# Kernel tuning notes

Hardware: AMD Instinct MI355X
Metric: run time of the kernel (lower is better)

## Reference

```python
import jax, jax.numpy as jnp
import numpy as np

B, N = 8, 1024
NFEAT, NHID, NHEADS, NCLASS, NLAYERS = 256, 64, 8, 256, 2
ALPHA = 0.2  # LeakyReLU slope inside GAT layers
OUTER_SLOPE = 0.01  # F.leaky_relu default on concatenated heads
NEG = -9e15


def setup_inputs() -> dict:
    key = jax.random.key(0)
    ks = jax.random.split(key, 8)
    x = jax.random.normal(ks[0], (B, N, NFEAT), jnp.float32)
    adj = jax.random.randint(ks[1], (B, N, N), 0, 2).astype(jnp.int32)
    mask = jax.random.randint(ks[2], (B, N), 0, 2).astype(jnp.int32)
    W_att = (jax.random.normal(ks[3], (NHEADS, NFEAT, NHID), jnp.float32) * 0.05)
    a_att = (jax.random.normal(ks[4], (NHEADS, 2 * NHID), jnp.float32) * 0.05)
    W_out = (jax.random.normal(ks[5], (NHID * NHEADS, NCLASS), jnp.float32) * 0.05)
    a_out = (jax.random.normal(ks[6], (2 * NCLASS,), jnp.float32) * 0.05)
    ln_w = jnp.ones((NCLASS,), jnp.float32)
    ln_b = jnp.zeros((NCLASS,), jnp.float32)
    return {"x": x, "adj": adj, "mask": mask, "W_att": W_att, "a_att": a_att,
            "W_out": W_out, "a_out": a_out, "ln_w": ln_w, "ln_b": ln_b}


def _layernorm(x, w, b):
    mu = jnp.mean(x, axis=-1, keepdims=True)
    var = jnp.mean(jnp.square(x - mu), axis=-1, keepdims=True)
    return (x - mu) * jax.lax.rsqrt(var + 1e-5) * w + b


def _gat_forward(x, adj_pos, maskb, W_att, a_att, W_out, a_out, ln_w, ln_b):
    for _ in range(NLAYERS):
        # multi-head GAT layers (concat=True): e_ij = leakyrelu(f1_i + f2_j)
        h = jnp.einsum('bnf,hfo->bhno', x, W_att)            # [B,H,N,F]
        f1 = jnp.einsum('bhno,ho->bhn', h, a_att[:, :NHID])  # [B,H,N]
        f2 = jnp.einsum('bhno,ho->bhn', h, a_att[:, NHID:])
        e = jax.nn.leaky_relu(f1[:, :, :, None] + f2[:, :, None, :], ALPHA)
        att = jax.nn.softmax(jnp.where(adj_pos[:, None], e, NEG), axis=-1)
        hp = jax.nn.elu(jnp.einsum('bhnm,bhmo->bhno', att, h))
        y = jax.nn.leaky_relu(
            hp.transpose(0, 2, 1, 3).reshape(B, N, NHEADS * NHID), OUTER_SLOPE)
        # out attention layer (concat=False)
        ho = y @ W_out                                        # [B,N,C]
        g1 = ho @ a_out[:NCLASS]                              # [B,N]
        g2 = ho @ a_out[NCLASS:]
        eo = jax.nn.leaky_relu(g1[:, :, None] + g2[:, None, :], ALPHA)
        ao = jax.nn.softmax(jnp.where(adj_pos, eo, NEG), axis=-1)
        x = x + jax.nn.elu(jnp.einsum('bnm,bmo->bno', ao, ho))
        x = jnp.where(maskb, 0.0, x)
        x = _layernorm(x, ln_w, ln_b)
    return jax.nn.relu(x), jax.nn.relu(x[:, 0, :])


def reference(x, adj, mask, W_att, a_att, W_out, a_out, ln_w, ln_b):
    adj_pos = adj > 0
    maskb = (mask == 0)[:, :, None]
    return _gat_forward(x, adj_pos, maskb, W_att, a_att, W_out, a_out, ln_w, ln_b)
```

## Files before the change

### kernel.cpp

```cpp
#include <hip/hip_runtime.h>
#include <hip/hip_bf16.h>
#include <math.h>

#define BB 8
#define NN 1024
#define FF 256
#define HH 8
#define OO 64
#define CC 256

typedef __attribute__((ext_vector_type(8))) short short8;
typedef __attribute__((ext_vector_type(4))) short s16x4;
typedef __attribute__((ext_vector_type(4))) float f32x4;
typedef unsigned long long u64;

__device__ __forceinline__ short bf16s(float f) {
    __hip_bfloat16 h = __float2bfloat16(f);
    return *reinterpret_cast<short*>(&h);
}

__global__ void k_prep(const int* __restrict__ adj, const float* __restrict__ x,
                       const float* __restrict__ Wa, const float* __restrict__ Wo,
                       u64* __restrict__ adjbit, __hip_bfloat16* __restrict__ xbf,
                       __hip_bfloat16* __restrict__ WaT, __hip_bfloat16* __restrict__ WoT) {
    int bid = blockIdx.x, t = threadIdx.x;
    if (bid < 32768) {
        int i = bid * 256 + t;
        u64 m = __ballot(adj[i] > 0);
        if ((t & 63) == 0) adjbit[i >> 6] = m;
    } else if (bid < 32768 + 8192) {
        int i = (bid - 32768) * 256 + t;
        xbf[i] = __float2bfloat16(x[i]);
    } else {
        int i = (bid - 32768 - 8192) * 256 + t;
        if (i < 131072) {
            int hd = i >> 14, o = (i >> 8) & 63, f = i & 255;
            WaT[i] = __float2bfloat16(Wa[hd * 16384 + f * 64 + o]);
        } else {
            int j = i - 131072;
            int c = j >> 9, k = j & 511;
            WoT[j] = __float2bfloat16(Wo[k * 256 + c]);
        }
    }
}

__global__ void k_proj_mfma(const __hip_bfloat16* __restrict__ xbf,
                            const __hip_bfloat16* __restrict__ WaT,
                            const float* __restrict__ aatt,
                            __hip_bfloat16* __restrict__ hF,
                            float* __restrict__ f1, float* __restrict__ f2) {
    int tile = blockIdx.x, hd = blockIdx.y;
    int t = threadIdx.x, lane = t & 63, w = t >> 6;
    int r0 = tile * 64;
    int b = r0 >> 10;
    int n0 = r0 & 1023;
    int bh = b * HH + hd;
    int al = lane & 15, ah = lane >> 4;
    const __hip_bfloat16* xrow = xbf + (size_t)(r0 + w * 16 + al) * FF;
    const __hip_bfloat16* Wb = WaT + (size_t)hd * OO * FF;
    f32x4 z4 = {0.f, 0.f, 0.f, 0.f};
    f32x4 acc[4] = {z4, z4, z4, z4};
    for (int k0 = 0; k0 < FF; k0 += 32) {
        int k = k0 + ah * 8;
        short8 af = *(const short8*)&xrow[k];
#pragma unroll
        for (int cf = 0; cf < 4; ++cf) {
            int col = cf * 16 + al;
            short8 bf = *(const short8*)&Wb[(size_t)col * FF + k];
            acc[cf] = __builtin_amdgcn_mfma_f32_16x16x32_bf16(af, bf, acc[cf], 0, 0, 0);
        }
    }
    int kw = tile & 15;
    int half = w >> 1;
    int hg = (w & 1) * 2 + (ah >> 1);
    int q0 = (ah & 1) * 4;
#pragma unroll
    for (int cf = 0; cf < 4; ++cf) {
        size_t base = ((((size_t)bh * 16 + kw) * 4 + cf) * 2 + half) * 512 +
                      (hg * 16 + al) * 8 + q0;
        s16x4 v;
#pragma unroll
        for (int r = 0; r < 4; ++r) v[r] = bf16s(acc[cf][r]);
        *(s16x4*)&hF[base] = v;
    }
    int nb = n0 + w * 16 + ah * 4;
    float p1[4] = {0.f, 0.f, 0.f, 0.f}, p2[4] = {0.f, 0.f, 0.f, 0.f};
#pragma unroll
    for (int cf = 0; cf < 4; ++cf) {
        int col = cf * 16 + al;
        float a1 = aatt[hd * 2 * OO + col];
        float a2 = aatt[hd * 2 * OO + OO + col];
#pragma unroll
        for (int r = 0; r < 4; ++r) {
            p1[r] += acc[cf][r] * a1;
            p2[r] += acc[cf][r] * a2;
        }
    }
#pragma unroll
    for (int off = 1; off < 16; off <<= 1) {
#pragma unroll
        for (int r = 0; r < 4; ++r) {
            p1[r] += __shfl_xor(p1[r], off);
            p2[r] += __shfl_xor(p2[r], off);
        }
    }
    if (al == 0) {
#pragma unroll
        for (int r = 0; r < 4; ++r) {
            f1[(size_t)bh * NN + nb + r] = p1[r];
            f2[(size_t)bh * NN + nb + r] = p2[r];
        }
    }
}

__global__ void k_att_fused(const u64* __restrict__ adjbit, const float* __restrict__ f1,
                            const float* __restrict__ f2,
                            const __hip_bfloat16* __restrict__ hF,
                            __hip_bfloat16* __restrict__ ybf) {
    int orig = blockIdx.x;
    int wgid = (orig & 7) * 128 + (orig >> 3);
    int bh = wgid >> 4;
    int n0 = (wgid & 15) * 64;
    int b = bh >> 3, hd = bh & 7;
    int t = threadIdx.x, lane = t & 63, w = t >> 6;
    __shared__ float Qs[1024], Ss[1024];
    __shared__ u64 bits[64 * 17];
    const float* f2b = f2 + (size_t)bh * NN;
    for (int j = t; j < 1024; j += 256) {
        float v = f2b[j];
        Qs[j] = __expf(v);
        Ss[j] = __expf(0.2f * v);
    }
    for (int e = t; e < 1024; e += 256) {
        int rr = e >> 4, c = e & 15;
        bits[rr * 17 + c] = adjbit[((size_t)b * NN + n0 + rr) * 16 + c];
    }
    int g = lane >> 4, r = lane & 15;
    int row = w * 16 + r;
    float fl = f1[(size_t)bh * NN + n0 + row];
    float P = __expf(fl), R = __expf(0.2f * fl);
    __syncthreads();
    const __hip_bfloat16* hFb = hF + (size_t)bh * 16 * 4 * 2 * 512 + lane * 8;
    f32x4 z4 = {0.f, 0.f, 0.f, 0.f};
    f32x4 acc[4] = {z4, z4, z4, z4};
    float ps = 0.f;
    int c0 = g * 8;
    auto BUILD = [&](int kw, short8& a0, short8& a1) {
        int k0 = kw * 64;
        u64 m = bits[row * 17 + kw];
        unsigned bl0 = (unsigned)(m >> c0) & 0xffu;
        unsigned bl1 = (unsigned)((m >> 32) >> c0) & 0xffu;
        f32x4 qa0 = *(const f32x4*)&Qs[k0 + c0];
        f32x4 qb0 = *(const f32x4*)&Qs[k0 + c0 + 4];
        f32x4 sa0 = *(const f32x4*)&Ss[k0 + c0];
        f32x4 sb0 = *(const f32x4*)&Ss[k0 + c0 + 4];
        f32x4 qa1 = *(const f32x4*)&Qs[k0 + 32 + c0];
        f32x4 qb1 = *(const f32x4*)&Qs[k0 + 32 + c0 + 4];
        f32x4 sa1 = *(const f32x4*)&Ss[k0 + 32 + c0];
        f32x4 sb1 = *(const f32x4*)&Ss[k0 + 32 + c0 + 4];
#pragma unroll
        for (int e = 0; e < 4; ++e) {
            float v0 = ((bl0 >> e) & 1) ? fmaxf(P * qa0[e], R * sa0[e]) : 0.f;
            float v1 = ((bl0 >> (4 + e)) & 1) ? fmaxf(P * qb0[e], R * sb0[e]) : 0.f;
            float v2 = ((bl1 >> e) & 1) ? fmaxf(P * qa1[e], R * sa1[e]) : 0.f;
            float v3 = ((bl1 >> (4 + e)) & 1) ? fmaxf(P * qb1[e], R * sb1[e]) : 0.f;
            ps += (v0 + v1) + (v2 + v3);
            a0[e] = bf16s(v0);
            a0[4 + e] = bf16s(v1);
            a1[e] = bf16s(v2);
            a1[4 + e] = bf16s(v3);
        }
    };
    auto LOADB = [&](int kw, short8* d0, short8* d1) {
#pragma unroll
        for (int cf = 0; cf < 4; ++cf) {
            const __hip_bfloat16* blk = hFb + ((size_t)(kw * 4 + cf) * 2) * 512;
            d0[cf] = *(const short8*)&blk[0];
            d1[cf] = *(const short8*)&blk[512];
        }
    };
    short8 pA0[4], pA1[4], pB0[4], pB1[4];
    LOADB(0, pA0, pA1);
    for (int kp = 0; kp < 8; ++kp) {
        short8 a0, a1;
        BUILD(2 * kp, a0, a1);
        LOADB(2 * kp + 1, pB0, pB1);
#pragma unroll
        for (int cf = 0; cf < 4; ++cf) {
            acc[cf] = __builtin_amdgcn_mfma_f32_16x16x32_bf16(a0, pA0[cf], acc[cf], 0, 0, 0);
            acc[cf] = __builtin_amdgcn_mfma_f32_16x16x32_bf16(a1, pA1[cf], acc[cf], 0, 0, 0);
        }
        BUILD(2 * kp + 1, a0, a1);
        if (kp < 7) LOADB(2 * kp + 2, pA0, pA1);
#pragma unroll
        for (int cf = 0; cf < 4; ++cf) {
            acc[cf] = __builtin_amdgcn_mfma_f32_16x16x32_bf16(a0, pB0[cf], acc[cf], 0, 0, 0);
            acc[cf] = __builtin_amdgcn_mfma_f32_16x16x32_bf16(a1, pB1[cf], acc[cf], 0, 0, 0);
        }
    }
    ps += __shfl_xor(ps, 16);
    ps += __shfl_xor(ps, 32);
#pragma unroll
    for (int rr = 0; rr < 4; ++rr) {
        int rloc = g * 4 + rr;
        float dn = __shfl(ps, rloc);
        float ids = 1.0f / dn;
        int nrow = n0 + w * 16 + rloc;
#pragma unroll
        for (int cf = 0; cf < 4; ++cf) {
            float v = acc[cf][rr] * ids;
            float e = v > 0.f ? v : expm1f(v);
            float yv = e > 0.f ? e : 0.01f * e;
            ybf[((size_t)b * NN + nrow) * 512 + hd * OO + cf * 16 + r] =
                __float2bfloat16(yv);
        }
    }
}

__global__ void k_outproj_mfma(const __hip_bfloat16* __restrict__ ybf,
                               const __hip_bfloat16* __restrict__ WoT,
                               const float* __restrict__ ao,
                               __hip_bfloat16* __restrict__ hoF,
                               float* __restrict__ g1, float* __restrict__ g2) {
    int orig = blockIdx.x;
    int tile = (orig & 7) * 64 + (orig >> 3);
    int t = threadIdx.x, lane = t & 63, w = t >> 6;
    int r0 = tile * 16;
    int b = r0 >> 10;
    __shared__ __align__(16) __hip_bfloat16 As[16][520];
    __shared__ float pg1[8][16], pg2[8][16];
    for (int e = t; e < 1024; e += 512) {
        int row = e >> 6, k8 = (e & 63) * 8;
        *(short8*)&As[row][k8] = *(const short8*)&ybf[(size_t)(r0 + row) * 512 + k8];
    }
    __syncthreads();
    int al = lane & 15, ah = lane >> 4;
    f32x4 z4 = {0.f, 0.f, 0.f, 0.f};
    f32x4 acc[2] = {z4, z4};
    for (int k0 = 0; k0 < 512; k0 += 32) {
        int k = k0 + ah * 8;
        short8 a0 = *(const short8*)&As[al][k];
#pragma unroll
        for (int cf = 0; cf < 2; ++cf) {
            int col = w * 32 + cf * 16 + al;
            short8 bf = *(const short8*)&WoT[(size_t)col * 512 + k];
            acc[cf] = __builtin_amdgcn_mfma_f32_16x16x32_bf16(a0, bf, acc[cf], 0, 0, 0);
        }
    }
    int kw = (tile & 63) >> 2;
    int half = (tile >> 1) & 1;
    int hg0 = (tile & 1) * 2 + (ah >> 1);
    int q0 = (ah & 1) * 4;
    float q1[4] = {0.f, 0.f, 0.f, 0.f};
    float q2[4] = {0.f, 0.f, 0.f, 0.f};
#pragma unroll
    for (int cf = 0; cf < 2; ++cf) {
        int col = w * 32 + cf * 16 + al;
        int cfB = w * 2 + cf;
        float a1v = ao[col], a2v = ao[CC + col];
        size_t base = ((((size_t)b * 16 + kw) * 16 + cfB) * 2 + half) * 512;
        s16x4 v0;
#pragma unroll
        for (int r = 0; r < 4; ++r) {
            v0[r] = bf16s(acc[cf][r]);
            q1[r] += acc[cf][r] * a1v;
            q2[r] += acc[cf][r] * a2v;
        }
        *(s16x4*)&hoF[base + (hg0 * 16 + al) * 8 + q0] = v0;
    }
#pragma unroll
    for (int off = 1; off < 16; off <<= 1) {
#pragma unroll
        for (int j = 0; j < 4; ++j) {
            q1[j] += __shfl_xor(q1[j], off);
            q2[j] += __shfl_xor(q2[j], off);
        }
    }
    if (al == 0) {
#pragma unroll
        for (int j = 0; j < 4; ++j) {
            pg1[w][ah * 4 + j] = q1[j];
            pg2[w][ah * 4 + j] = q2[j];
        }
    }
    __syncthreads();
    if (t < 16) {
        float s1 = 0.f, s2 = 0.f;
#pragma unroll
        for (int ww = 0; ww < 8; ++ww) {
            s1 += pg1[ww][t];
            s2 += pg2[ww][t];
        }
        g1[r0 + t] = s1;
        g2[r0 + t] = s2;
    }
}

__global__ void k_out_fused(const u64* __restrict__ adjbit, const float* __restrict__ g1,
                            const float* __restrict__ g2,
                            const __hip_bfloat16* __restrict__ hoF,
                            const float* __restrict__ xin, const int* __restrict__ mask,
                            const float* __restrict__ lw, const float* __restrict__ lb,
                            float* __restrict__ xout, __hip_bfloat16* __restrict__ xbfout,
                            float* __restrict__ outf, int final_) {
    int orig = blockIdx.x;
    int wgid = (orig & 7) * 64 + (orig >> 3);
    int b = wgid >> 6;
    int n0 = (wgid & 63) * 16;
    int t = threadIdx.x, lane = t & 63, w = t >> 6;
    __shared__ float Qs[1024], Ss[1024];
    __shared__ u64 bits[16 * 17];
    __shared__ float lns[8][16], lnq[8][16];
    const float* g2b = g2 + (size_t)b * NN;
    for (int j = t; j < 1024; j += 512) {
        float v = g2b[j];
        Qs[j] = __expf(v);
        Ss[j] = __expf(0.2f * v);
    }
    if (t < 256) {
        int rr = t >> 4, c = t & 15;
        bits[rr * 17 + c] = adjbit[((size_t)b * NN + n0 + rr) * 16 + c];
    }
    int g = lane >> 4, r = lane & 15;
    float gl = g1[(size_t)b * NN + n0 + r];
    float P = __expf(gl);
    float R = __expf(0.2f * gl);
    __syncthreads();
    const __hip_bfloat16* hoFb = hoF + (size_t)b * 16 * 16 * 2 * 512 + lane * 8;
    f32x4 z4 = {0.f, 0.f, 0.f, 0.f};
    f32x4 acc[2] = {z4, z4};
    float ps = 0.f;
    int c0 = g * 8;
    auto BUILD = [&](int kw, short8& a0, short8& a1) {
        int k0 = kw * 64;
        u64 m = bits[r * 17 + kw];
        unsigned bl0 = (unsigned)(m >> c0) & 0xffu;
        unsigned bl1 = (unsigned)((m >> 32) >> c0) & 0xffu;
        f32x4 qa0 = *(const f32x4*)&Qs[k0 + c0];
        f32x4 qb0 = *(const f32x4*)&Qs[k0 + c0 + 4];
        f32x4 sa0 = *(const f32x4*)&Ss[k0 + c0];
        f32x4 sb0 = *(const f32x4*)&Ss[k0 + c0 + 4];
        f32x4 qa1 = *(const f32x4*)&Qs[k0 + 32 + c0];
        f32x4 qb1 = *(const f32x4*)&Qs[k0 + 32 + c0 + 4];
        f32x4 sa1 = *(const f32x4*)&Ss[k0 + 32 + c0];
        f32x4 sb1 = *(const f32x4*)&Ss[k0 + 32 + c0 + 4];
#pragma unroll
        for (int e = 0; e < 4; ++e) {
            float v0 = ((bl0 >> e) & 1) ? fmaxf(P * qa0[e], R * sa0[e]) : 0.f;
            float v1 = ((bl0 >> (4 + e)) & 1) ? fmaxf(P * qb0[e], R * sb0[e]) : 0.f;
            float v2 = ((bl1 >> e) & 1) ? fmaxf(P * qa1[e], R * sa1[e]) : 0.f;
            float v3 = ((bl1 >> (4 + e)) & 1) ? fmaxf(P * qb1[e], R * sb1[e]) : 0.f;
            ps += (v0 + v1) + (v2 + v3);
            a0[e] = bf16s(v0);
            a0[4 + e] = bf16s(v1);
            a1[e] = bf16s(v2);
            a1[4 + e] = bf16s(v3);
        }
    };
    auto LOADB = [&](int kw, short8* d0, short8* d1) {
#pragma unroll
        for (int cf = 0; cf < 2; ++cf) {
            int cfB = w * 2 + cf;
            const __hip_bfloat16* blk = hoFb + ((size_t)(kw * 16 + cfB) * 2) * 512;
            d0[cf] = *(const short8*)&blk[0];
            d1[cf] = *(const short8*)&blk[512];
        }
    };
    short8 pA0[2], pA1[2], pB0[2], pB1[2];
    LOADB(0, pA0, pA1);
    for (int kp = 0; kp < 8; ++kp) {
        short8 a0, a1;
        BUILD(2 * kp, a0, a1);
        LOADB(2 * kp + 1, pB0, pB1);
#pragma unroll
        for (int cf = 0; cf < 2; ++cf) {
            acc[cf] = __builtin_amdgcn_mfma_f32_16x16x32_bf16(a0, pA0[cf], acc[cf], 0, 0, 0);
            acc[cf] = __builtin_amdgcn_mfma_f32_16x16x32_bf16(a1, pA1[cf], acc[cf], 0, 0, 0);
        }
        BUILD(2 * kp + 1, a0, a1);
        if (kp < 7) LOADB(2 * kp + 2, pA0, pA1);
#pragma unroll
        for (int cf = 0; cf < 2; ++cf) {
            acc[cf] = __builtin_amdgcn_mfma_f32_16x16x32_bf16(a0, pB0[cf], acc[cf], 0, 0, 0);
            acc[cf] = __builtin_amdgcn_mfma_f32_16x16x32_bf16(a1, pB1[cf], acc[cf], 0, 0, 0);
        }
    }
    ps += __shfl_xor(ps, 16);
    ps += __shfl_xor(ps, 32);
    float tv[4][2];
#pragma unroll
    for (int rr = 0; rr < 4; ++rr) {
        int rloc = g * 4 + rr;
        float dn = __shfl(ps, rloc);
        float ids = 1.0f / dn;
        int nrow = n0 + rloc;
        int mk = mask[b * NN + nrow];
        size_t rowo = ((size_t)b * NN + nrow) * CC;
        float s1 = 0.f, s2 = 0.f;
#pragma unroll
        for (int cf = 0; cf < 2; ++cf) {
            int col = w * 32 + cf * 16 + r;
            float v = acc[cf][rr] * ids;
            float e = v > 0.f ? v : expm1f(v);
            float tvv = (mk == 0) ? 0.f : (xin[rowo + col] + e);
            tv[rr][cf] = tvv;
            s1 += tvv;
            s2 += tvv * tvv;
        }
#pragma unroll
        for (int off = 1; off < 16; off <<= 1) {
            s1 += __shfl_xor(s1, off);
            s2 += __shfl_xor(s2, off);
        }
        if (r == 0) {
            lns[w][rloc] = s1;
            lnq[w][rloc] = s2;
        }
    }
    __syncthreads();
#pragma unroll
    for (int rr = 0; rr < 4; ++rr) {
        int rloc = g * 4 + rr;
        int nrow = n0 + rloc;
        size_t rowo = ((size_t)b * NN + nrow) * CC;
        float su = 0.f, sq = 0.f;
#pragma unroll
        for (int ww = 0; ww < 8; ++ww) {
            su += lns[ww][rloc];
            sq += lnq[ww][rloc];
        }
        float mu = su * (1.0f / CC);
        float var = sq * (1.0f / CC) - mu * mu;
        float rstd = rsqrtf(var + 1e-5f);
#pragma unroll
        for (int cf = 0; cf < 2; ++cf) {
            int col = w * 32 + cf * 16 + r;
            float ln = (tv[rr][cf] - mu) * rstd * lw[col] + lb[col];
            if (final_) {
                float rv = ln > 0.f ? ln : 0.f;
                outf[rowo + col] = rv;
                if (nrow == 0) outf[(size_t)BB * NN * CC + b * CC + col] = rv;
            } else {
                xout[rowo + col] = ln;
                xbfout[rowo + col] = __float2bfloat16(ln);
            }
        }
    }
}

extern "C" void kernel_launch(void* const* d_in, const int* in_sizes, int n_in,
                              void* d_out, int out_size, void* d_ws, size_t ws_size,
                              hipStream_t stream) {
    const float* x = (const float*)d_in[0];
    const int* adj = (const int*)d_in[1];
    const int* mask = (const int*)d_in[2];
    const float* W_att = (const float*)d_in[3];
    const float* a_att = (const float*)d_in[4];
    const float* W_out = (const float*)d_in[5];
    const float* a_out = (const float*)d_in[6];
    const float* ln_w = (const float*)d_in[7];
    const float* ln_b = (const float*)d_in[8];
    float* out = (float*)d_out;

    float* ws = (float*)d_ws;
    float* xbuf = ws;
    float* xbfr = xbuf + 2097152;
    float* f1   = xbfr + 2097152;
    float* f2   = f1 + 65536;
    float* g1   = f2 + 65536;
    float* g2   = g1 + 8192;
    float* p    = g2 + 8192;
    __hip_bfloat16* xbf = (__hip_bfloat16*)xbfr;
    __hip_bfloat16* hF  = (__hip_bfloat16*)p;
    __hip_bfloat16* ybf = (__hip_bfloat16*)(p + 2097152);
    __hip_bfloat16* hoF = (__hip_bfloat16*)(p + 4194304);
    __hip_bfloat16* WaT = (__hip_bfloat16*)(p + 5242880);
    __hip_bfloat16* WoT = (__hip_bfloat16*)(p + 5308416);
    u64* adjbit = (u64*)(p + 5373952);

    k_prep<<<32768 + 8192 + 1024, 256, 0, stream>>>(adj, x, W_att, W_out,
                                                    adjbit, xbf, WaT, WoT);

    for (int layer = 0; layer < 2; ++layer) {
        const float* xin_l = layer ? xbuf : x;
        k_proj_mfma<<<dim3(128, 8), 256, 0, stream>>>(xbf, WaT, a_att, hF, f1, f2);
        k_att_fused<<<1024, 256, 0, stream>>>(adjbit, f1, f2, hF, ybf);
        k_outproj_mfma<<<512, 512, 0, stream>>>(ybf, WoT, a_out, hoF, g1, g2);
        k_out_fused<<<512, 512, 0, stream>>>(adjbit, g1, g2, hoF, xin_l, mask,
                                             ln_w, ln_b, xbuf, xbf, out, layer == 1);
    }
}
```

Before: 197.2 us.

## Split out-attention K dimension across waves with LDS tree reduction

Changes the work split in the fused output-attention kernel. Before, each of the 8 waves built the full attention A-fragments over all 16 key chunks and did MFMAs for 32 output columns. Now each wave covers 4 key chunks (a split-K) and 128 columns, so each A-fragment build is done once per wave rather than redundantly by all 8 waves. Partial accumulators and row sums are combined through a two-stage shared-memory tree reduction, and only 2 waves then run the ELU/LayerNorm epilogue. The cost is extra LDS traffic, more __syncthreads, higher register pressure from 8 accumulators, loss of the explicit B-load double buffering, and an epilogue that runs on fewer waves.

New measurement: 208.5 us. 1.06x slower.

```diff
diff --git a/kernel.cpp b/kernel.cpp
--- a/kernel.cpp
+++ b/kernel.cpp
@@ -308,9 +308,12 @@
     int b = wgid >> 6;
     int n0 = (wgid & 63) * 16;
     int t = threadIdx.x, lane = t & 63, w = t >> 6;
+    int ch = w & 1, kq = w >> 1;
     __shared__ float Qs[1024], Ss[1024];
     __shared__ u64 bits[16 * 17];
-    __shared__ float lns[8][16], lnq[8][16];
+    __shared__ f32x4 accbuf[4][8][64];
+    __shared__ float psbuf[4][64];
+    __shared__ float lns[2][16], lnq[2][16];
     const float* g2b = g2 + (size_t)b * NN;
     for (int j = t; j < 1024; j += 512) {
         float v = g2b[j];
@@ -328,7 +331,7 @@
     __syncthreads();
     const __hip_bfloat16* hoFb = hoF + (size_t)b * 16 * 16 * 2 * 512 + lane * 8;
     f32x4 z4 = {0.f, 0.f, 0.f, 0.f};
-    f32x4 acc[2] = {z4, z4};
+    f32x4 acc[8] = {z4, z4, z4, z4, z4, z4, z4, z4};
     float ps = 0.f;
     int c0 = g * 8;
     auto BUILD = [&](int kw, short8& a0, short8& a1) {
@@ -357,92 +360,100 @@
             a1[4 + e] = bf16s(v3);
         }
     };
-    auto LOADB = [&](int kw, short8* d0, short8* d1) {
-#pragma unroll
-        for (int cf = 0; cf < 2; ++cf) {
-            int cfB = w * 2 + cf;
+#pragma unroll
+    for (int kwl = 0; kwl < 4; ++kwl) {
+        int kw = kq * 4 + kwl;
+        short8 a0, a1;
+        BUILD(kw, a0, a1);
+#pragma unroll
+        for (int cf = 0; cf < 8; ++cf) {
+            int cfB = ch * 8 + cf;
             const __hip_bfloat16* blk = hoFb + ((size_t)(kw * 16 + cfB) * 2) * 512;
-            d0[cf] = *(const short8*)&blk[0];
-            d1[cf] = *(const short8*)&blk[512];
-        }
-    };
-    short8 pA0[2], pA1[2], pB0[2], pB1[2];
-    LOADB(0, pA0, pA1);
-    for (int kp = 0; kp < 8; ++kp) {
-        short8 a0, a1;
-        BUILD(2 * kp, a0, a1);
-        LOADB(2 * kp + 1, pB0, pB1);
-#pragma unroll
-        for (int cf = 0; cf < 2; ++cf) {
-            acc[cf] = __builtin_amdgcn_mfma_f32_16x16x32_bf16(a0, pA0[cf], acc[cf], 0, 0, 0);
-            acc[cf] = __builtin_amdgcn_mfma_f32_16x16x32_bf16(a1, pA1[cf], acc[cf], 0, 0, 0);
-        }
-        BUILD(2 * kp + 1, a0, a1);
-        if (kp < 7) LOADB(2 * kp + 2, pA0, pA1);
-#pragma unroll
-        for (int cf = 0; cf < 2; ++cf) {
-            acc[cf] = __builtin_amdgcn_mfma_f32_16x16x32_bf16(a0, pB0[cf], acc[cf], 0, 0, 0);
-            acc[cf] = __builtin_amdgcn_mfma_f32_16x16x32_bf16(a1, pB1[cf], acc[cf], 0, 0, 0);
+            short8 b0 = *(const short8*)&blk[0];
+            short8 b1 = *(const short8*)&blk[512];
+            acc[cf] = __builtin_amdgcn_mfma_f32_16x16x32_bf16(a0, b0, acc[cf], 0, 0, 0);
+            acc[cf] = __builtin_amdgcn_mfma_f32_16x16x32_bf16(a1, b1, acc[cf], 0, 0, 0);
         }
     }
     ps += __shfl_xor(ps, 16);
     ps += __shfl_xor(ps, 32);
-    float tv[4][2];
-#pragma unroll
-    for (int rr = 0; rr < 4; ++rr) {
-        int rloc = g * 4 + rr;
-        float dn = __shfl(ps, rloc);
-        float ids = 1.0f / dn;
-        int nrow = n0 + rloc;
-        int mk = mask[b * NN + nrow];
-        size_t rowo = ((size_t)b * NN + nrow) * CC;
-        float s1 = 0.f, s2 = 0.f;
-#pragma unroll
-        for (int cf = 0; cf < 2; ++cf) {
-            int col = w * 32 + cf * 16 + r;
-            float v = acc[cf][rr] * ids;
-            float e = v > 0.f ? v : expm1f(v);
-            float tvv = (mk == 0) ? 0.f : (xin[rowo + col] + e);
-            tv[rr][cf] = tvv;
-            s1 += tvv;
-            s2 += tvv * tvv;
-        }
-#pragma unroll
-        for (int off = 1; off < 16; off <<= 1) {
-            s1 += __shfl_xor(s1, off);
-            s2 += __shfl_xor(s2, off);
-        }
-        if (r == 0) {
-            lns[w][rloc] = s1;
-            lnq[w][rloc] = s2;
-        }
-    }
-    __syncthreads();
-#pragma unroll
-    for (int rr = 0; rr < 4; ++rr) {
-        int rloc = g * 4 + rr;
-        int nrow = n0 + rloc;
-        size_t rowo = ((size_t)b * NN + nrow) * CC;
-        float su = 0.f, sq = 0.f;
-#pragma unroll
-        for (int ww = 0; ww < 8; ++ww) {
-            su += lns[ww][rloc];
-            sq += lnq[ww][rloc];
-        }
-        float mu = su * (1.0f / CC);
-        float var = sq * (1.0f / CC) - mu * mu;
-        float rstd = rsqrtf(var + 1e-5f);
-#pragma unroll
-        for (int cf = 0; cf < 2; ++cf) {
-            int col = w * 32 + cf * 16 + r;
-            float ln = (tv[rr][cf] - mu) * rstd * lw[col] + lb[col];
-            if (final_) {
-                float rv = ln > 0.f ? ln : 0.f;
-                outf[rowo + col] = rv;
-                if (nrow == 0) outf[(size_t)BB * NN * CC + b * CC + col] = rv;
-            } else {
-                xout[rowo + col] = ln;
-                xbfout[rowo + col] = __float2bfloat16(ln);
+    if (w >= 4) {
+#pragma unroll
+        for (int cf = 0; cf < 8; ++cf) accbuf[w - 4][cf][lane] = acc[cf];
+        psbuf[w - 4][lane] = ps;
+    }
+    __syncthreads();
+    if (w < 4) {
+#pragma unroll
+        for (int cf = 0; cf < 8; ++cf) acc[cf] += accbuf[w][cf][lane];
+        ps += psbuf[w][lane];
+    }
+    __syncthreads();
+    if (w == 2 || w == 3) {
+#pragma unroll
+        for (int cf = 0; cf < 8; ++cf) accbuf[w - 2][cf][lane] = acc[cf];
+        psbuf[w - 2][lane] = ps;
+    }
+    __syncthreads();
+    float tv[4][8];
+    if (w < 2) {
+#pragma unroll
+        for (int cf = 0; cf < 8; ++cf) acc[cf] += accbuf[w][cf][lane];
+        ps += psbuf[w][lane];
+#pragma unroll
+        for (int rr = 0; rr < 4; ++rr) {
+            int rloc = g * 4 + rr;
+            float dn = __shfl(ps, rloc);
+            float ids = 1.0f / dn;
+            int nrow = n0 + rloc;
+            int mk = mask[b * NN + nrow];
+            size_t rowo = ((size_t)b * NN + nrow) * CC;
+            float s1 = 0.f, s2 = 0.f;
+#pragma unroll
+            for (int cf = 0; cf < 8; ++cf) {
+                int col = w * 128 + cf * 16 + r;
+                float v = acc[cf][rr] * ids;
+                float e = v > 0.f ? v : expm1f(v);
+                float tvv = (mk == 0) ? 0.f : (xin[rowo + col] + e);
+                tv[rr][cf] = tvv;
+                s1 += tvv;
+                s2 += tvv * tvv;
+            }
+#pragma unroll
+            for (int off = 1; off < 16; off <<= 1) {
+                s1 += __shfl_xor(s1, off);
+                s2 += __shfl_xor(s2, off);
+            }
+            if (r == 0) {
+                lns[w][rloc] = s1;
+                lnq[w][rloc] = s2;
+            }
+        }
+    }
+    __syncthreads();
+    if (w < 2) {
+#pragma unroll
+        for (int rr = 0; rr < 4; ++rr) {
+            int rloc = g * 4 + rr;
+            int nrow = n0 + rloc;
+            size_t rowo = ((size_t)b * NN + nrow) * CC;
+            float su = lns[0][rloc] + lns[1][rloc];
+            float sq = lnq[0][rloc] + lnq[1][rloc];
+            float mu = su * (1.0f / CC);
+            float var = sq * (1.0f / CC) - mu * mu;
+            float rstd = rsqrtf(var + 1e-5f);
+#pragma unroll
+            for (int cf = 0; cf < 8; ++cf) {
+                int col = w * 128 + cf * 16 + r;
+                float ln = (tv[rr][cf] - mu) * rstd * lw[col] + lb[col];
+                if (final_) {
+                    float rv = ln > 0.f ? ln : 0.f;
+                    outf[rowo + col] = rv;
+                    if (nrow == 0) outf[(size_t)BB * NN * CC + b * CC + col] = rv;
+                } else {
+                    xout[rowo + col] = ln;
+                    xbfout[rowo + col] = __float2bfloat16(ln);
+                }
             }
         }
     }
```
